# Kernel tuning notes

Hardware: AMD Instinct MI355X
Metric: run time of the kernel (lower is better)

## Reference

```python
import jax, jax.numpy as jnp
import numpy as np

G = 16          # GroupNorm groups
EPS = 1e-5


def setup_inputs() -> dict:
    key = jax.random.key(0)
    ks = jax.random.split(key, 6)
    B, C, H, W = 2, 256, 96, 96
    O = 256
    x = jax.random.normal(ks[0], (B, C, H, W), dtype=jnp.float32)
    offset = jax.random.normal(ks[1], (B, 18, H, W), dtype=jnp.float32)
    mask = jax.random.uniform(ks[2], (B, 9, H, W), dtype=jnp.float32)
    fan_in = C * 9
    weight = jax.random.normal(ks[3], (O, C, 3, 3), dtype=jnp.float32) / np.sqrt(fan_in)
    bias = jnp.zeros((O,), dtype=jnp.float32)
    gamma = jnp.ones((O,), dtype=jnp.float32)
    beta = jnp.zeros((O,), dtype=jnp.float32)
    return {"x": x, "offset": offset, "mask": mask, "weight": weight,
            "bias": bias, "gamma": gamma, "beta": beta}


def _mdcn_gn(x, offset, mask, weight, bias, gamma, beta):
    B, C, H, W = x.shape
    O = weight.shape[0]
    K = 9
    # offsets: mmcv layout [y0,x0,y1,x1,...] per kernel point k = kh*3+kw
    off = offset.reshape(B, K, 2, H, W)
    off_y, off_x = off[:, :, 0], off[:, :, 1]            # [B,K,H,W]
    ky = (jnp.arange(K) // 3 - 1).astype(x.dtype)        # kernel dy, pad=1
    kx = (jnp.arange(K) % 3 - 1).astype(x.dtype)
    hh = jnp.arange(H, dtype=x.dtype)[:, None]
    ww = jnp.arange(W, dtype=x.dtype)[None, :]
    py = hh[None, None] + ky[:, None, None] + off_y      # [B,K,H,W] sample y
    px = ww[None, None] + kx[:, None, None] + off_x      # [B,K,H,W] sample x

    y0 = jnp.floor(py)
    x0 = jnp.floor(px)
    dy = py - y0
    dx = px - x0
    y0i = y0.astype(jnp.int32)
    x0i = x0.astype(jnp.int32)

    xf = x.reshape(B, C, H * W)

    def gather(yi, xi):
        # zero-padded bilinear corner: out-of-range corners contribute 0
        valid = ((yi >= 0) & (yi < H) & (xi >= 0) & (xi < W)).astype(x.dtype)
        yc = jnp.clip(yi, 0, H - 1)
        xc = jnp.clip(xi, 0, W - 1)
        idx = (yc * W + xc).reshape(B, 1, K * H * W)
        v = jnp.take_along_axis(xf, idx, axis=2).reshape(B, C, K, H, W)
        return v * valid.reshape(B, 1, K, H, W)

    w00 = ((1 - dy) * (1 - dx))[:, None]                 # [B,1,K,H,W]
    w01 = ((1 - dy) * dx)[:, None]
    w10 = (dy * (1 - dx))[:, None]
    w11 = (dy * dx)[:, None]
    val = (gather(y0i, x0i) * w00 + gather(y0i, x0i + 1) * w01 +
           gather(y0i + 1, x0i) * w10 + gather(y0i + 1, x0i + 1) * w11)
    val = val * mask[:, None]                            # modulation [B,C,K,H,W]

    out = jnp.einsum('ock,bckhw->bohw', weight.reshape(O, C, K), val)
    out = out + bias[None, :, None, None]

    # GroupNorm(16, O)
    xg = out.reshape(B, G, O // G, H, W)
    mean = xg.mean(axis=(2, 3, 4), keepdims=True)
    var = jnp.mean((xg - mean) ** 2, axis=(2, 3, 4), keepdims=True)
    xn = ((xg - mean) * jax.lax.rsqrt(var + EPS)).reshape(B, O, H, W)
    return xn * gamma[None, :, None, None] + beta[None, :, None, None]


def reference(x, offset, mask, weight, bias, gamma, beta):
    return _mdcn_gn(x, offset, mask, weight, bias, gamma, beta)
```

## Files before the change

### kernel.cpp

```cpp
#include <hip/hip_runtime.h>
#include <hip/hip_fp16.h>

typedef _Float16 f16;
typedef __attribute__((ext_vector_type(2))) _Float16 h2v;
typedef __attribute__((ext_vector_type(8))) _Float16 f16x8;
typedef __attribute__((ext_vector_type(4))) float f32x4;

#define HW_    9216
#define PADP   8
#define XP_    112
#define XPXP_  12544
#define NSTEP  72
#define NMT    288
#define XT_BYTES   12845056
#define BMAT_BYTES 1179648
#define ATILE_B    294912
#define OUTH_BYTES 9437184
#define PART_BYTES 73728

union U4 { uint4 u; h2v h[4]; f16x8 v; f16 f[8]; };
union U1 { unsigned u; h2v h; };
union UO { ushort4 s; f16 f[4]; };

__global__ __launch_bounds__(256) void k_prep_x(const float* __restrict__ x, f16* __restrict__ xT) {
    __shared__ float tile[64 * 97];
    int blk = blockIdx.x;
    int cg  = blk & 3;
    int y   = (blk >> 2) % 96;
    int b   = blk / 384;
    int t   = threadIdx.x;
    const float* src = x + (((size_t)(b*256 + cg*64))*96 + y)*96;
    for (int e = t; e < 6144; e += 256) {
        int c = e / 96, wcol = e - c*96;
        tile[c*97 + wcol] = src[(size_t)c*HW_ + wcol];
    }
    __syncthreads();
    f16* dst = xT + ((size_t)b*XPXP_ + (size_t)(y+PADP)*XP_ + PADP)*256 + cg*64;
    for (int e = t; e < 6144; e += 256) {
        int wcol = e >> 6, c = e & 63;
        dst[(size_t)wcol*256 + c] = (f16)tile[c*97 + wcol];
    }
}

__global__ __launch_bounds__(256) void k_prep_w(const float* __restrict__ wgt, f16* __restrict__ bmat) {
    int id = blockIdx.x*256 + threadIdx.x;
    int o = id / 2304;
    int rem = id - o*2304;
    int c = rem / 9;
    int k = rem - c*9;
    int s  = k*8 + (c >> 5);
    int nw = o >> 6, fn = (o >> 4) & 3, r = o & 15;
    int kq = (c >> 3) & 3, e = c & 7;
    bmat[(size_t)s*8192 + nw*2048 + fn*512 + (kq*16 + r)*8 + e] = (f16)wgt[id];
}

__global__ __launch_bounds__(256, 6) void k_sample(
        const f16* __restrict__ xT, const float* __restrict__ offs,
        const float* __restrict__ maskp, f16* __restrict__ Ag, int mt0, int nblk)
{
    __shared__ int   geo_i[64];
    __shared__ uint4 geo_w[64];

    int blk0 = blockIdx.x;
    int blk  = (blk0 & 7)*(nblk >> 3) + (blk0 >> 3);
    int mtl  = blk / 9;
    int k    = blk - mtl*9;
    int mt   = mt0 + mtl;
    int b    = mt / 144;

    int tid = threadIdx.x;
    if (tid < 64) {
        int hw = mt*64 + tid - b*HW_;
        int h = hw / 96, w = hw - h*96;
        float offy = offs[((size_t)b*18 + 2*k    )*HW_ + hw];
        float offx = offs[((size_t)b*18 + 2*k + 1)*HW_ + hw];
        float mv   = maskp[((size_t)b*9 + k)*HW_ + hw];
        int ky = k/3 - 1, kx = k - (k/3)*3 - 1;
        float py = (float)(h + ky) + offy;
        float px = (float)(w + kx) + offx;
        py = fminf(fmaxf(py, -7.5f), 102.4f);
        px = fminf(fmaxf(px, -7.5f), 102.4f);
        float y0 = floorf(py), x0 = floorf(px);
        float dy = py - y0,   dx = px - x0;
        geo_i[tid] = (((int)y0 + PADP)*XP_ + ((int)x0 + PADP)) << 9;
        float w00v = (1.f-dy)*(1.f-dx)*mv, w01v = (1.f-dy)*dx*mv;
        float w10v = dy*(1.f-dx)*mv,       w11v = dy*dx*mv;
        U1 p0, p1, p2, p3;
        p0.h = h2v{(f16)w00v, (f16)w00v};
        p1.h = h2v{(f16)w01v, (f16)w01v};
        p2.h = h2v{(f16)w10v, (f16)w10v};
        p3.h = h2v{(f16)w11v, (f16)w11v};
        geo_w[tid] = uint4{p0.u, p1.u, p2.u, p3.u};
    }
    __syncthreads();

    const char* xbC = (const char*)xT + (size_t)b*XPXP_*512;
    char* dst = (char*)Ag + (size_t)mtl*ATILE_B;

    #pragma unroll
    for (int j = 0; j < 8; ++j) {
        int item = tid + j*256;
        int row = item >> 5, chunk = item & 31;
        const char* p = xbC + geo_i[row] + (chunk << 4);
        U4 t0, t1, t2, t3, oo;
        t0.u = *(const uint4*)(p);
        t1.u = *(const uint4*)(p + 512);
        t2.u = *(const uint4*)(p + XP_*512);
        t3.u = *(const uint4*)(p + XP_*512 + 512);
        U4 w4; w4.u = geo_w[row];
        h2v w00 = w4.h[0], w01 = w4.h[1], w10 = w4.h[2], w11 = w4.h[3];
        #pragma unroll
        for (int q = 0; q < 4; ++q)
            oo.h[q] = w00*t0.h[q] + w01*t1.h[q] + w10*t2.h[q] + w11*t3.h[q];
        int s = k*8 + (chunk >> 2);
        size_t off = (size_t)(row >> 5)*147456 + (size_t)s*2048
                   + ((row >> 4) & 1)*1024 + (((chunk & 3)*16 + (row & 15)) << 4);
        *(uint4*)(dst + off) = oo.u;
    }
}

#define MFMA16(a,b,c) __builtin_amdgcn_mfma_f32_16x16x32_f16(a,b,c,0,0,0)

#define LOADS(A0,A1,B0,B1,B2,B3, s_) do { \
    const char* pa_ = aB + (size_t)(s_)*2048; \
    const char* pb_ = bB + (size_t)(s_)*16384; \
    A0 = *(const uint4*)(pa_); \
    A1 = *(const uint4*)(pa_ + 1024); \
    B0 = *(const uint4*)(pb_); \
    B1 = *(const uint4*)(pb_ + 1024); \
    B2 = *(const uint4*)(pb_ + 2048); \
    B3 = *(const uint4*)(pb_ + 3072); \
  } while (0)

#define MMS(A0,A1,B0,B1,B2,B3) do { \
    U4 xa0, xa1, xb; xa0.u = A0; xa1.u = A1; \
    xb.u = B0; acc[0][0] = MFMA16(xa0.v, xb.v, acc[0][0]); acc[1][0] = MFMA16(xa1.v, xb.v, acc[1][0]); \
    xb.u = B1; acc[0][1] = MFMA16(xa0.v, xb.v, acc[0][1]); acc[1][1] = MFMA16(xa1.v, xb.v, acc[1][1]); \
    xb.u = B2; acc[0][2] = MFMA16(xa0.v, xb.v, acc[0][2]); acc[1][2] = MFMA16(xa1.v, xb.v, acc[1][2]); \
    xb.u = B3; acc[0][3] = MFMA16(xa0.v, xb.v, acc[0][3]); acc[1][3] = MFMA16(xa1.v, xb.v, acc[1][3]); \
  } while (0)

__global__ __launch_bounds__(64) void k_gemm(
        const f16* __restrict__ Ag, const f16* __restrict__ bmat,
        const float* __restrict__ bias, f16* __restrict__ outh,
        float* __restrict__ part, int mt0, int nwv)
{
    int w0 = blockIdx.x;
    int w  = (w0 & 7)*(nwv >> 3) + (w0 >> 3);
    int mw = w >> 2, nw = w & 3;
    int lane = threadIdx.x;

    const char* aB = (const char*)Ag + (size_t)mw*147456 + lane*16;
    const char* bB = (const char*)bmat + nw*4096 + lane*16;

    f32x4 acc[2][4];
    #pragma unroll
    for (int i = 0; i < 2; ++i)
        #pragma unroll
        for (int j = 0; j < 4; ++j) acc[i][j] = (f32x4){0.f,0.f,0.f,0.f};

    uint4 a00,a01,b00,b01,b02,b03;
    uint4 a10,a11,b10,b11,b12,b13;
    uint4 a20,a21,b20,b21,b22,b23;

    LOADS(a00,a01,b00,b01,b02,b03, 0);
    LOADS(a10,a11,b10,b11,b12,b13, 1);
    LOADS(a20,a21,b20,b21,b22,b23, 2);

    for (int s = 0; s < 69; s += 3) {
        MMS(a00,a01,b00,b01,b02,b03);  LOADS(a00,a01,b00,b01,b02,b03, s+3);
        MMS(a10,a11,b10,b11,b12,b13);  LOADS(a10,a11,b10,b11,b12,b13, s+4);
        MMS(a20,a21,b20,b21,b22,b23);  LOADS(a20,a21,b20,b21,b22,b23, s+5);
    }
    MMS(a00,a01,b00,b01,b02,b03);
    MMS(a10,a11,b10,b11,b12,b13);
    MMS(a20,a21,b20,b21,b22,b23);

    int mwg = mt0*2 + mw;
    int b   = mwg / 288;
    int hwb = mwg*32 - b*HW_;
    int ol  = lane & 15;
    int qr  = (lane >> 4) << 2;
    #pragma unroll
    for (int fm = 0; fm < 2; ++fm) {
        #pragma unroll
        for (int fn = 0; fn < 4; ++fn) {
            int o = nw*64 + fn*16 + ol;
            float bv = bias[o];
            f32x4 a = acc[fm][fn];
            a[0] += bv; a[1] += bv; a[2] += bv; a[3] += bv;
            acc[fm][fn] = a;
            UO ov;
            ov.f[0] = (f16)a[0]; ov.f[1] = (f16)a[1];
            ov.f[2] = (f16)a[2]; ov.f[3] = (f16)a[3];
            *(ushort4*)(outh + ((size_t)(b*256 + o))*HW_ + hwb + fm*16 + qr) = ov.s;
        }
    }
    #pragma unroll
    for (int fn = 0; fn < 4; ++fn) {
        float s1 = 0.f, s2 = 0.f;
        #pragma unroll
        for (int fm = 0; fm < 2; ++fm) {
            f32x4 a = acc[fm][fn];
            s1 += a[0]+a[1]+a[2]+a[3];
            s2 += a[0]*a[0]+a[1]*a[1]+a[2]*a[2]+a[3]*a[3];
        }
        #pragma unroll
        for (int m = 32; m > 0; m >>= 1) {
            s1 += __shfl_xor(s1, m);
            s2 += __shfl_xor(s2, m);
        }
        if (lane == 0) {
            part[((size_t)mwg*16 + nw*4 + fn)*2]     = s1;
            part[((size_t)mwg*16 + nw*4 + fn)*2 + 1] = s2;
        }
    }
}

__global__ __launch_bounds__(256) void k_finalize(const float* __restrict__ part, float* __restrict__ stats) {
    int bg = blockIdx.x, b = bg >> 4, g = bg & 15;
    float s1 = 0.f, s2 = 0.f;
    for (int j = threadIdx.x; j < 288; j += 256) {
        const float* p = part + ((size_t)(b*288 + j)*16 + g)*2;
        s1 += p[0]; s2 += p[1];
    }
    __shared__ float a1[256], a2[256];
    a1[threadIdx.x] = s1; a2[threadIdx.x] = s2;
    __syncthreads();
    for (int off = 128; off > 0; off >>= 1) {
        if (threadIdx.x < off) { a1[threadIdx.x] += a1[threadIdx.x+off]; a2[threadIdx.x] += a2[threadIdx.x+off]; }
        __syncthreads();
    }
    if (threadIdx.x == 0) {
        float inv_n = 1.f/147456.f;
        float mean = a1[0]*inv_n;
        float var  = fmaxf(a2[0]*inv_n - mean*mean, 0.f);
        stats[bg*2]   = mean;
        stats[bg*2+1] = rsqrtf(var + 1e-5f);
    }
}

__global__ __launch_bounds__(256) void k_norm(const f16* __restrict__ outh, float* __restrict__ out,
                                              const float* __restrict__ stats,
                                              const float* __restrict__ gamma, const float* __restrict__ beta) {
    int i8 = blockIdx.x*256 + threadIdx.x;
    int p  = i8 / 1152;
    int o  = p & 255;
    float mean = stats[(p>>4)*2], rstd = stats[(p>>4)*2 + 1];
    float ga = gamma[o]*rstd, be = beta[o] - mean*rstd*gamma[o];
    U4 v; v.u = ((const uint4*)outh)[i8];
    float4 o0, o1;
    o0.x = (float)v.f[0]*ga + be; o0.y = (float)v.f[1]*ga + be;
    o0.z = (float)v.f[2]*ga + be; o0.w = (float)v.f[3]*ga + be;
    o1.x = (float)v.f[4]*ga + be; o1.y = (float)v.f[5]*ga + be;
    o1.z = (float)v.f[6]*ga + be; o1.w = (float)v.f[7]*ga + be;
    ((float4*)out)[i8*2]     = o0;
    ((float4*)out)[i8*2 + 1] = o1;
}

extern "C" void kernel_launch(void* const* d_in, const int* in_sizes, int n_in,
                              void* d_out, int out_size, void* d_ws, size_t ws_size,
                              hipStream_t stream) {
    const float* x      = (const float*)d_in[0];
    const float* offset = (const float*)d_in[1];
    const float* mask   = (const float*)d_in[2];
    const float* weight = (const float*)d_in[3];
    const float* bias   = (const float*)d_in[4];
    const float* gamma  = (const float*)d_in[5];
    const float* beta   = (const float*)d_in[6];
    float* out = (float*)d_out;

    char* ws = (char*)d_ws;
    f16*   xT    = (f16*)ws;
    f16*   bmat  = (f16*)(ws + XT_BYTES);
    float* part  = (float*)(ws + XT_BYTES + BMAT_BYTES);
    float* stats = (float*)(ws + XT_BYTES + BMAT_BYTES + PART_BYTES);
    f16*   outh  = (f16*)(ws + XT_BYTES + BMAT_BYTES + PART_BYTES + 256);
    char*  Ag    = ws + XT_BYTES + BMAT_BYTES + PART_BYTES + 256 + OUTH_BYTES;

    size_t needA = (size_t)NMT * ATILE_B;
    size_t base  = (size_t)XT_BYTES + BMAT_BYTES + PART_BYTES + 256 + OUTH_BYTES;
    size_t avail = ws_size > base ? ws_size - base : 0;
    int P = (avail >= needA) ? 1 : ((avail >= needA/2) ? 2 : 4);

    (void)hipMemsetAsync(xT, 0, XT_BYTES, stream);
    k_prep_x<<<768, 256, 0, stream>>>(x, xT);
    k_prep_w<<<2304, 256, 0, stream>>>(weight, bmat);
    int mtn = NMT / P;
    for (int p = 0; p < P; ++p) {
        k_sample<<<mtn*9, 256, 0, stream>>>(xT, offset, mask, (f16*)Ag, p*mtn, mtn*9);
        k_gemm<<<mtn*8, 64, 0, stream>>>((f16*)Ag, bmat, bias, outh, part, p*mtn, mtn*8);
    }
    k_finalize<<<32, 256, 0, stream>>>(part, stats);
    k_norm<<<2304, 256, 0, stream>>>(outh, out, stats, gamma, beta);
}
```

Before: 97.57 us.

## Enlarge GEMM per-wave M tile from 32 to 96 rows to reuse B fragments

Each single-wave GEMM block now computes a 96x64 output tile (6x4 MFMA accumulators) instead of 32x64. Each loaded B fragment then feeds three times as many MFMAs, which cuts global B traffic and the number of waves, and with them the GroupNorm partial-sum count that k_finalize reads. The trade-off is far more registers per wave (launch_bounds(64,1)) and fewer waves in flight (768 vs 2304), so latency hiding and occupancy may suffer.

```diff
diff --git a/kernel.cpp b/kernel.cpp
--- a/kernel.cpp
+++ b/kernel.cpp
@@ -15,8 +15,9 @@
 #define XT_BYTES   12845056
 #define BMAT_BYTES 1179648
 #define ATILE_B    294912
+#define A32_B      147456
 #define OUTH_BYTES 9437184
-#define PART_BYTES 73728
+#define PART_BYTES 24576
 
 union U4 { uint4 u; h2v h[4]; f16x8 v; f16 f[8]; };
 union U1 { unsigned u; h2v h; };
@@ -113,7 +114,7 @@
         for (int q = 0; q < 4; ++q)
             oo.h[q] = w00*t0.h[q] + w01*t1.h[q] + w10*t2.h[q] + w11*t3.h[q];
         int s = k*8 + (chunk >> 2);
-        size_t off = (size_t)(row >> 5)*147456 + (size_t)s*2048
+        size_t off = (size_t)(row >> 5)*A32_B + (size_t)s*2048
                    + ((row >> 4) & 1)*1024 + (((chunk & 3)*16 + (row & 15)) << 4);
         *(uint4*)(dst + off) = oo.u;
     }
@@ -121,87 +122,98 @@
 
 #define MFMA16(a,b,c) __builtin_amdgcn_mfma_f32_16x16x32_f16(a,b,c,0,0,0)
 
-#define LOADS(A0,A1,B0,B1,B2,B3, s_) do { \
+#define DECLSET(P) uint4 A##P##0,A##P##1,A##P##2,A##P##3,A##P##4,A##P##5, \
+                         B##P##0,B##P##1,B##P##2,B##P##3
+
+#define LOADSET(P, s_) do { \
     const char* pa_ = aB + (size_t)(s_)*2048; \
     const char* pb_ = bB + (size_t)(s_)*16384; \
-    A0 = *(const uint4*)(pa_); \
-    A1 = *(const uint4*)(pa_ + 1024); \
-    B0 = *(const uint4*)(pb_); \
-    B1 = *(const uint4*)(pb_ + 1024); \
-    B2 = *(const uint4*)(pb_ + 2048); \
-    B3 = *(const uint4*)(pb_ + 3072); \
+    A##P##0 = *(const uint4*)(pa_); \
+    A##P##1 = *(const uint4*)(pa_ + 1024); \
+    A##P##2 = *(const uint4*)(pa_ + A32_B); \
+    A##P##3 = *(const uint4*)(pa_ + A32_B + 1024); \
+    A##P##4 = *(const uint4*)(pa_ + 2*A32_B); \
+    A##P##5 = *(const uint4*)(pa_ + 2*A32_B + 1024); \
+    B##P##0 = *(const uint4*)(pb_); \
+    B##P##1 = *(const uint4*)(pb_ + 1024); \
+    B##P##2 = *(const uint4*)(pb_ + 2048); \
+    B##P##3 = *(const uint4*)(pb_ + 3072); \
   } while (0)
 
-#define MMS(A0,A1,B0,B1,B2,B3) do { \
-    U4 xa0, xa1, xb; xa0.u = A0; xa1.u = A1; \
-    xb.u = B0; acc[0][0] = MFMA16(xa0.v, xb.v, acc[0][0]); acc[1][0] = MFMA16(xa1.v, xb.v, acc[1][0]); \
-    xb.u = B1; acc[0][1] = MFMA16(xa0.v, xb.v, acc[0][1]); acc[1][1] = MFMA16(xa1.v, xb.v, acc[1][1]); \
-    xb.u = B2; acc[0][2] = MFMA16(xa0.v, xb.v, acc[0][2]); acc[1][2] = MFMA16(xa1.v, xb.v, acc[1][2]); \
-    xb.u = B3; acc[0][3] = MFMA16(xa0.v, xb.v, acc[0][3]); acc[1][3] = MFMA16(xa1.v, xb.v, acc[1][3]); \
+#define MMROW(P, jm, Areg) do { \
+    U4 xa_, xb_; xa_.u = Areg; \
+    xb_.u = B##P##0; acc[jm][0] = MFMA16(xa_.v, xb_.v, acc[jm][0]); \
+    xb_.u = B##P##1; acc[jm][1] = MFMA16(xa_.v, xb_.v, acc[jm][1]); \
+    xb_.u = B##P##2; acc[jm][2] = MFMA16(xa_.v, xb_.v, acc[jm][2]); \
+    xb_.u = B##P##3; acc[jm][3] = MFMA16(xa_.v, xb_.v, acc[jm][3]); \
   } while (0)
 
-__global__ __launch_bounds__(64) void k_gemm(
+#define MMSET(P) do { \
+    MMROW(P, 0, A##P##0); MMROW(P, 1, A##P##1); MMROW(P, 2, A##P##2); \
+    MMROW(P, 3, A##P##3); MMROW(P, 4, A##P##4); MMROW(P, 5, A##P##5); \
+  } while (0)
+
+__global__ __launch_bounds__(64, 1) void k_gemm(
         const f16* __restrict__ Ag, const f16* __restrict__ bmat,
         const float* __restrict__ bias, f16* __restrict__ outh,
-        float* __restrict__ part, int mt0, int nwv)
+        float* __restrict__ part, int row0, int nwv)
 {
     int w0 = blockIdx.x;
     int w  = (w0 & 7)*(nwv >> 3) + (w0 >> 3);
-    int mw = w >> 2, nw = w & 3;
+    int mwl = w >> 2, nw = w & 3;
     int lane = threadIdx.x;
 
-    const char* aB = (const char*)Ag + (size_t)mw*147456 + lane*16;
+    const char* aB = (const char*)Ag + (size_t)mwl*(3*A32_B) + lane*16;
     const char* bB = (const char*)bmat + nw*4096 + lane*16;
 
-    f32x4 acc[2][4];
+    f32x4 acc[6][4];
     #pragma unroll
-    for (int i = 0; i < 2; ++i)
+    for (int i = 0; i < 6; ++i)
         #pragma unroll
         for (int j = 0; j < 4; ++j) acc[i][j] = (f32x4){0.f,0.f,0.f,0.f};
 
-    uint4 a00,a01,b00,b01,b02,b03;
-    uint4 a10,a11,b10,b11,b12,b13;
-    uint4 a20,a21,b20,b21,b22,b23;
-
-    LOADS(a00,a01,b00,b01,b02,b03, 0);
-    LOADS(a10,a11,b10,b11,b12,b13, 1);
-    LOADS(a20,a21,b20,b21,b22,b23, 2);
+    DECLSET(0); DECLSET(1); DECLSET(2);
+
+    LOADSET(0, 0);
+    LOADSET(1, 1);
+    LOADSET(2, 2);
 
     for (int s = 0; s < 69; s += 3) {
-        MMS(a00,a01,b00,b01,b02,b03);  LOADS(a00,a01,b00,b01,b02,b03, s+3);
-        MMS(a10,a11,b10,b11,b12,b13);  LOADS(a10,a11,b10,b11,b12,b13, s+4);
-        MMS(a20,a21,b20,b21,b22,b23);  LOADS(a20,a21,b20,b21,b22,b23, s+5);
-    }
-    MMS(a00,a01,b00,b01,b02,b03);
-    MMS(a10,a11,b10,b11,b12,b13);
-    MMS(a20,a21,b20,b21,b22,b23);
-
-    int mwg = mt0*2 + mw;
-    int b   = mwg / 288;
-    int hwb = mwg*32 - b*HW_;
-    int ol  = lane & 15;
-    int qr  = (lane >> 4) << 2;
+        MMSET(0);  LOADSET(0, s+3);
+        MMSET(1);  LOADSET(1, s+4);
+        MMSET(2);  LOADSET(2, s+5);
+    }
+    MMSET(0);
+    MMSET(1);
+    MMSET(2);
+
+    int grow = row0 + mwl*96;
+    int mwg  = grow / 96;
+    int b    = grow / HW_;
+    int hwb  = grow - b*HW_;
+    int ol   = lane & 15;
+    int qr   = (lane >> 4) << 2;
     #pragma unroll
-    for (int fm = 0; fm < 2; ++fm) {
+    for (int jm = 0; jm < 6; ++jm) {
         #pragma unroll
         for (int fn = 0; fn < 4; ++fn) {
             int o = nw*64 + fn*16 + ol;
             float bv = bias[o];
-            f32x4 a = acc[fm][fn];
+            f32x4 a = acc[jm][fn];
             a[0] += bv; a[1] += bv; a[2] += bv; a[3] += bv;
-            acc[fm][fn] = a;
+            acc[jm][fn] = a;
             UO ov;
             ov.f[0] = (f16)a[0]; ov.f[1] = (f16)a[1];
             ov.f[2] = (f16)a[2]; ov.f[3] = (f16)a[3];
-            *(ushort4*)(outh + ((size_t)(b*256 + o))*HW_ + hwb + fm*16 + qr) = ov.s;
+            *(ushort4*)(outh + ((size_t)(b*256 + o))*HW_ + hwb + jm*16 + qr) = ov.s;
         }
     }
     #pragma unroll
     for (int fn = 0; fn < 4; ++fn) {
         float s1 = 0.f, s2 = 0.f;
         #pragma unroll
-        for (int fm = 0; fm < 2; ++fm) {
-            f32x4 a = acc[fm][fn];
+        for (int jm = 0; jm < 6; ++jm) {
+            f32x4 a = acc[jm][fn];
             s1 += a[0]+a[1]+a[2]+a[3];
             s2 += a[0]*a[0]+a[1]*a[1]+a[2]*a[2]+a[3]*a[3];
         }
@@ -220,9 +232,9 @@
 __global__ __launch_bounds__(256) void k_finalize(const float* __restrict__ part, float* __restrict__ stats) {
     int bg = blockIdx.x, b = bg >> 4, g = bg & 15;
     float s1 = 0.f, s2 = 0.f;
-    for (int j = threadIdx.x; j < 288; j += 256) {
-        const float* p = part + ((size_t)(b*288 + j)*16 + g)*2;
-        s1 += p[0]; s2 += p[1];
+    if (threadIdx.x < 96) {
+        const float* p = part + ((size_t)(b*96 + threadIdx.x)*16 + g)*2;
+        s1 = p[0]; s2 = p[1];
     }
     __shared__ float a1[256], a2[256];
     a1[threadIdx.x] = s1; a2[threadIdx.x] = s2;
@@ -287,9 +299,10 @@
     k_prep_x<<<768, 256, 0, stream>>>(x, xT);
     k_prep_w<<<2304, 256, 0, stream>>>(weight, bmat);
     int mtn = NMT / P;
+    int nwv = 768 / P;
     for (int p = 0; p < P; ++p) {
         k_sample<<<mtn*9, 256, 0, stream>>>(xT, offset, mask, (f16*)Ag, p*mtn, mtn*9);
-        k_gemm<<<mtn*8, 64, 0, stream>>>((f16*)Ag, bmat, bias, outh, part, p*mtn, mtn*8);
+        k_gemm<<<nwv, 64, 0, stream>>>((f16*)Ag, bmat, bias, outh, part, p*mtn*64, nwv);
     }
     k_finalize<<<32, 256, 0, stream>>>(part, stats);
     k_norm<<<2304, 256, 0, stream>>>(outh, out, stats, gamma, beta);
```

New measurement: 87.36 us. 1.12x faster.
